# Kernel tuning notes

Measured on AMD Instinct MI355X. Metric: run time of the kernel, lower is better.

The kernel has to match this reference:

```python
import jax, jax.numpy as jnp
import numpy as np

N_PER_G = 100  # nodes per graph


def setup_inputs() -> dict:
    key = jax.random.key(0)
    ks = jax.random.split(key, 12)
    N, G, E = 100000, 1000, 1600000
    ninp, nout, K, H, H2 = 3, 10, 5, 64, 32
    x = jax.random.normal(ks[0], (N, ninp), jnp.float32)
    # within-graph random edges (contiguous node blocks per graph)
    epg = E // G
    gid = jnp.arange(E, dtype=jnp.int32) // epg
    src = jax.random.randint(ks[1], (E,), 0, N_PER_G, jnp.int32) + gid * N_PER_G
    dst = jax.random.randint(ks[2], (E,), 0, N_PER_G, jnp.int32) + gid * N_PER_G
    edge_index = jnp.stack([src, dst])
    batch = (jnp.arange(N, dtype=jnp.int32) // N_PER_G)
    lambda_max = 1.5 + 0.5 * jax.random.uniform(ks[3], (G,), jnp.float32)
    s = 0.05
    W1 = jax.random.normal(ks[4], (K, ninp, H), jnp.float32) * s
    b1 = jnp.zeros((H,), jnp.float32)
    W2 = jax.random.normal(ks[5], (K, H, H), jnp.float32) * s
    b2 = jnp.zeros((H,), jnp.float32)
    W3 = jax.random.normal(ks[6], (K, H, H), jnp.float32) * s
    b3 = jnp.zeros((H,), jnp.float32)
    bn_gamma = jnp.ones((H,), jnp.float32)
    bn_beta = jnp.zeros((H,), jnp.float32)
    bn_mean = jnp.zeros((H,), jnp.float32)
    bn_var = jnp.ones((H,), jnp.float32)
    fc1_w = jax.random.normal(ks[7], (H, H2), jnp.float32) * s
    fc1_b = jnp.zeros((H2,), jnp.float32)
    fc2_w = jax.random.normal(ks[8], (H2, nout), jnp.float32) * s
    fc2_b = jnp.zeros((nout,), jnp.float32)
    return dict(x=x, edge_index=edge_index, batch=batch, lambda_max=lambda_max,
                W1=W1, b1=b1, W2=W2, b2=b2, W3=W3, b3=b3,
                bn_gamma=bn_gamma, bn_beta=bn_beta, bn_mean=bn_mean, bn_var=bn_var,
                fc1_w=fc1_w, fc1_b=fc1_b, fc2_w=fc2_w, fc2_b=fc2_b)


def _cheb_conv(x, W, b, row, col, coef_edge, coef_loop):
    # PyG ChebConv with sym-normalized scaled Laplacian:
    # Lhat x = scatter_add(coef_edge * x[col] -> row) + coef_loop * x
    N = x.shape[0]
    def lhat(h):
        return jax.ops.segment_sum(coef_edge[:, None] * h[col], row,
                                   num_segments=N) + coef_loop[:, None] * h
    Tx0 = x
    out = Tx0 @ W[0]
    Tx1 = lhat(x)
    out = out + Tx1 @ W[1]
    for k in range(2, W.shape[0]):
        Tx2 = 2.0 * lhat(Tx1) - Tx0
        out = out + Tx2 @ W[k]
        Tx0, Tx1 = Tx1, Tx2
    return out + b


def reference(x, edge_index, batch, lambda_max,
              W1, b1, W2, b2, W3, b3,
              bn_gamma, bn_beta, bn_mean, bn_var,
              fc1_w, fc1_b, fc2_w, fc2_b):
    N = x.shape[0]
    G = lambda_max.shape[0]
    row, col = edge_index[0], edge_index[1]
    # sym Laplacian normalization, scaled by 2/lambda_max (per-graph)
    deg = jax.ops.segment_sum(jnp.ones_like(row, dtype=x.dtype), row, num_segments=N)
    dis = jnp.where(deg > 0, deg, 1.0) ** -0.5
    dis = jnp.where(deg > 0, dis, 0.0)
    lmax_e = lambda_max[batch[row]]
    coef_edge = -(2.0 / lmax_e) * dis[row] * dis[col]   # off-diagonal of Lhat
    coef_loop = 2.0 / lambda_max[batch] - 1.0           # diagonal of Lhat
    h = jax.nn.relu(_cheb_conv(x, W1, b1, row, col, coef_edge, coef_loop))
    h = jax.nn.relu(_cheb_conv(h, W2, b2, row, col, coef_edge, coef_loop))
    h = jax.nn.relu(_cheb_conv(h, W3, b3, row, col, coef_edge, coef_loop))
    # global mean pool over graphs
    sums = jax.ops.segment_sum(h, batch, num_segments=G)
    cnts = jax.ops.segment_sum(jnp.ones((N,), h.dtype), batch, num_segments=G)
    g = sums / jnp.maximum(cnts, 1.0)[:, None]
    # BatchNorm1d (eval mode, running stats), eps=1e-5
    g = (g - bn_mean) * jax.lax.rsqrt(bn_var + 1e-5) * bn_gamma + bn_beta
    g = jax.nn.relu(g @ fc1_w + fc1_b)
    return jax.nn.log_softmax(g @ fc2_w + fc2_b, axis=1)
```

## Files before the change

### kernel.cpp

```cpp
#include <hip/hip_runtime.h>

#define NPG 100
#define HF 64
#define SAT 136
#define CMW 29

typedef float  f4   __attribute__((ext_vector_type(4)));
typedef float  f16v __attribute__((ext_vector_type(16)));
typedef short  bf8  __attribute__((ext_vector_type(8)));

#define NB_T  (HF * SAT * 2)
#define OFF_MISC (2 * NB_T)
#define MISC_BYTES 2048
#define SMEM_BYTES (OFF_MISC + MISC_BYTES)

#define WT_TOTAL 46080

__device__ __forceinline__ unsigned short f2bf(float f) {
    unsigned u = __float_as_uint(f);
    u += 0x7fffu + ((u >> 16) & 1u);
    return (unsigned short)(u >> 16);
}
__device__ __forceinline__ unsigned cvt_pk_bf16(float lo, float hi) {
    unsigned r;
    asm("v_cvt_pk_bf16_f32 %0, %1, %2" : "=v"(r) : "v"(lo), "v"(hi));
    return r;
}
__device__ __forceinline__ f16v zerov16() {
    f16v z;
    #pragma unroll
    for (int i = 0; i < 16; i++) z[i] = 0.f;
    return z;
}

union BF8U { unsigned u[4]; bf8 b; };

__global__ void wconv(const float* __restrict__ W1, const float* __restrict__ W2,
                      const float* __restrict__ W3, unsigned short* __restrict__ ws)
{
    int idx = blockIdx.x * 256 + threadIdx.x;
    if (idx >= WT_TOTAL) return;
    float v;
    if (idx < 5120) {
        int k5 = idx >> 10, rem = idx & 1023, fo = rem >> 4, fi = rem & 15;
        v = (fi < 3) ? W1[(k5 * 3 + fi) * HF + fo] : 0.f;
    } else if (idx < 25600) {
        int j = idx - 5120;
        int k5 = j >> 12, rem = j & 4095, fo = rem >> 6, fi = rem & 63;
        v = W2[(k5 * HF + fi) * HF + fo];
    } else {
        int j = idx - 25600;
        int k5 = j >> 12, rem = j & 4095, fo = rem >> 6, fi = rem & 63;
        v = W3[(k5 * HF + fi) * HF + fo];
    }
    ws[idx] = f2bf(v);
}

__launch_bounds__(256, 2)
__global__ void chebreg(const float* __restrict__ x, const int* __restrict__ ei,
                        const float* __restrict__ lambda_max,
                        const unsigned short* __restrict__ Wt,
                        const float* __restrict__ b1, const float* __restrict__ b2,
                        const float* __restrict__ b3,
                        const float* __restrict__ bng, const float* __restrict__ bnb,
                        const float* __restrict__ bnm, const float* __restrict__ bnv,
                        const float* __restrict__ fc1w, const float* __restrict__ fc1b,
                        const float* __restrict__ fc2w, const float* __restrict__ fc2b,
                        float* __restrict__ out, int E_total, int epg)
{
    extern __shared__ char sm[];
    const int tid = threadIdx.x;
    const int g = blockIdx.x;
    const int ebase = g * epg, nbase = g * NPG;
    const int wg = tid >> 6, lane = tid & 63;
    const int l31 = lane & 31, hh = lane >> 5;
    const int nb = 32 * wg;
    const int np = nb + l31;
    const bool npv = (np < NPG);

    unsigned* Cm  = (unsigned*)sm;
    float* dis    = (float*)(sm + OFF_MISC);
    float* b_all  = (float*)(sm + OFF_MISC + 448);
    float* gvn    = (float*)(sm + OFF_MISC + 1216);
    float* zf     = (float*)(sm + OFF_MISC + 1472);
    float* logits = (float*)(sm + OFF_MISC + 1600);
    float* lsep   = (float*)(sm + OFF_MISC + 1664);

    const float lam = lambda_max[g];
    const float two_l = 2.0f / lam;
    const float cl = two_l - 1.0f;

    for (int i = tid; i < (128 * CMW) / 4; i += 256)
        ((f4*)Cm)[i] = (f4){0.f, 0.f, 0.f, 0.f};
    __syncthreads();
    for (int e = tid; e < epg; e += 256) {
        int r = ei[ebase + e] - nbase;
        int c = ei[E_total + ebase + e] - nbase;
        atomicAdd(&Cm[r * CMW + (c >> 2)], 1u << (8 * (c & 3)));
    }
    __syncthreads();
    if (tid < 112) {
        float dv = 0.f;
        if (tid < NPG) {
            unsigned s = 0;
            #pragma unroll
            for (int w = 0; w < 25; w++) {
                unsigned u = Cm[tid * CMW + w];
                s += (u & 255) + ((u >> 8) & 255) + ((u >> 16) & 255) + (u >> 24);
            }
            dv = s > 0 ? rsqrtf((float)s) : 0.f;
        }
        dis[tid] = dv;
    }
    if (tid < 192)
        b_all[tid] = (tid < 64) ? b1[tid] : (tid < 128) ? b2[tid - 64] : b3[tid - 128];
    __syncthreads();

    bf8 afT[7];
    {
        float base = npv ? (-two_l * dis[np]) : 0.f;
        #pragma unroll
        for (int Ks = 0; Ks < 7; Ks++) {
            int n0 = Ks * 16 + 8 * hh;
            unsigned w0 = npv ? Cm[np * CMW + (n0 >> 2)]     : 0u;
            unsigned w1 = npv ? Cm[np * CMW + (n0 >> 2) + 1] : 0u;
            float vv[8];
            #pragma unroll
            for (int j = 0; j < 8; j++) {
                int n = n0 + j;
                unsigned cnt = (((j < 4) ? w0 : w1) >> (8 * (n & 3))) & 255u;
                float v = base * (float)cnt * dis[n];
                if (npv && n == np) v += cl;
                vv[j] = v;
            }
            BF8U t;
            #pragma unroll
            for (int p = 0; p < 4; p++) t.u[p] = cvt_pk_bf16(vv[2 * p], vv[2 * p + 1]);
            afT[Ks] = t.b;
        }
    }
    __syncthreads();

    for (int i = tid; i < (2 * NB_T) / 16; i += 256)
        ((f4*)sm)[i] = (f4){0.f, 0.f, 0.f, 0.f};
    __syncthreads();

    unsigned prev[2][8], oldr[2][8];
    #pragma unroll
    for (int ct = 0; ct < 2; ct++)
        #pragma unroll
        for (int p = 0; p < 8; p++) prev[ct][p] = 0u;

    if (hh == 0 && npv) {
        float x0 = x[(nbase + np) * 3 + 0];
        float x1 = x[(nbase + np) * 3 + 1];
        float x2 = x[(nbase + np) * 3 + 2];
        prev[0][0] = cvt_pk_bf16(x0, x1);
        prev[0][1] = cvt_pk_bf16(x2, 0.f);
        *(unsigned short*)(sm + (0 * SAT + np) * 2) = (unsigned short)(prev[0][0] & 0xffff);
        *(unsigned short*)(sm + (1 * SAT + np) * 2) = (unsigned short)(prev[0][0] >> 16);
        *(unsigned short*)(sm + (2 * SAT + np) * 2) = (unsigned short)(prev[0][1] & 0xffff);
    }
    __syncthreads();

    f16v acc[2];
    int cur = 0;

    for (int L = 0; L < 3; L++) {
        const bool l0 = (L == 0);
        const unsigned short* Wl = l0 ? Wt : (Wt + (L == 1 ? 5120 : 25600));
        const int wstr = l0 ? 16 : 64;
        const int nKs  = l0 ? 1 : 4;
        acc[0] = zerov16();
        acc[1] = zerov16();

        auto TWreg = [&](int k5) {
            #pragma unroll
            for (int Ks = 0; Ks < 4; Ks++) {
                if (Ks < nKs) {
                    unsigned a0 = prev[Ks >> 1][4 * (Ks & 1) + 0];
                    unsigned b0 = prev[Ks >> 1][4 * (Ks & 1) + 2];
                    unsigned a1 = prev[Ks >> 1][4 * (Ks & 1) + 1];
                    unsigned b1v = prev[Ks >> 1][4 * (Ks & 1) + 3];
                    asm volatile("v_permlane32_swap_b32 %0, %1" : "+v"(a0), "+v"(b0));
                    asm volatile("v_permlane32_swap_b32 %0, %1" : "+v"(a1), "+v"(b1v));
                    BF8U bfr; bfr.u[0] = a0; bfr.u[1] = a1; bfr.u[2] = b0; bfr.u[3] = b1v;
                    #pragma unroll
                    for (int ct = 0; ct < 2; ct++) {
                        bf8 wf = *(const bf8*)(Wl + (k5 * 64 + 32 * ct + l31) * wstr
                                               + Ks * 16 + 8 * hh);
                        acc[ct] = __builtin_amdgcn_mfma_f32_32x32x16_bf16(wf, bfr.b, acc[ct], 0, 0, 0);
                    }
                }
            }
        };

        for (int s = 1; s <= 4; s++) {
            const char* bcur = sm + cur * NB_T;
            bf8 Af0[7], Af1[7];
            #pragma unroll
            for (int Ks = 0; Ks < 7; Ks++)
                Af0[Ks] = *(const bf8*)(bcur + ((0 + l31) * SAT + Ks * 16 + 8 * hh) * 2);
            if (!l0) {
                #pragma unroll
                for (int Ks = 0; Ks < 7; Ks++)
                    Af1[Ks] = *(const bf8*)(bcur + ((32 + l31) * SAT + Ks * 16 + 8 * hh) * 2);
            }
            f16v c0 = zerov16(), c1 = zerov16();
            #pragma unroll
            for (int Ks = 0; Ks < 7; Ks++)
                c0 = __builtin_amdgcn_mfma_f32_32x32x16_bf16(Af0[Ks], afT[Ks], c0, 0, 0, 0);
            if (!l0) {
                #pragma unroll
                for (int Ks = 0; Ks < 7; Ks++)
                    c1 = __builtin_amdgcn_mfma_f32_32x32x16_bf16(Af1[Ks], afT[Ks], c1, 0, 0, 0);
            }

            TWreg(s - 1);

            #pragma unroll
            for (int p = 0; p < 8; p++) {
                float ve = c0[2 * p], vo = c0[2 * p + 1];
                if (s >= 2) {
                    unsigned o = oldr[0][p];
                    ve = 2.f * ve - __uint_as_float(o << 16);
                    vo = 2.f * vo - __uint_as_float(o & 0xffff0000u);
                }
                oldr[0][p] = prev[0][p];
                prev[0][p] = cvt_pk_bf16(ve, vo);
            }
            if (!l0) {
                #pragma unroll
                for (int p = 0; p < 8; p++) {
                    float ve = c1[2 * p], vo = c1[2 * p + 1];
                    if (s >= 2) {
                        unsigned o = oldr[1][p];
                        ve = 2.f * ve - __uint_as_float(o << 16);
                        vo = 2.f * vo - __uint_as_float(o & 0xffff0000u);
                    }
                    oldr[1][p] = prev[1][p];
                    prev[1][p] = cvt_pk_bf16(ve, vo);
                }
            }

            if (s < 4) {
                char* bnx = sm + (cur ^ 1) * NB_T;
                if (l0) {
                    if (hh == 0) {
                        *(unsigned short*)(bnx + (0 * SAT + np) * 2) = (unsigned short)(prev[0][0] & 0xffff);
                        *(unsigned short*)(bnx + (1 * SAT + np) * 2) = (unsigned short)(prev[0][0] >> 16);
                        *(unsigned short*)(bnx + (2 * SAT + np) * 2) = (unsigned short)(prev[0][1] & 0xffff);
                    }
                } else {
                    #pragma unroll
                    for (int ct = 0; ct < 2; ct++) {
                        #pragma unroll
                        for (int p = 0; p < 8; p++) {
                            int fo = 32 * ct + ((2 * p) & 3) + 8 * (p >> 1) + 4 * hh;
                            *(unsigned short*)(bnx + (fo * SAT + np) * 2)       = (unsigned short)(prev[ct][p] & 0xffff);
                            *(unsigned short*)(bnx + ((fo + 1) * SAT + np) * 2) = (unsigned short)(prev[ct][p] >> 16);
                        }
                    }
                }
            }
            __syncthreads();
            cur ^= 1;
        }

        TWreg(4);

        if (L < 2) {
            const float* bl = b_all + L * 64;
            char* bt0 = sm + cur * NB_T;
            #pragma unroll
            for (int ct = 0; ct < 2; ct++) {
                #pragma unroll
                for (int p = 0; p < 8; p++) {
                    int fo = 32 * ct + ((2 * p) & 3) + 8 * (p >> 1) + 4 * hh;
                    float2 bb = *(const float2*)(bl + fo);
                    float ve = fmaxf(acc[ct][2 * p]     + bb.x, 0.f);
                    float vo = fmaxf(acc[ct][2 * p + 1] + bb.y, 0.f);
                    prev[ct][p] = cvt_pk_bf16(ve, vo);
                    *(unsigned short*)(bt0 + (fo * SAT + np) * 2)       = (unsigned short)(prev[ct][p] & 0xffff);
                    *(unsigned short*)(bt0 + ((fo + 1) * SAT + np) * 2) = (unsigned short)(prev[ct][p] >> 16);
                }
            }
            __syncthreads();
        } else {
            float* Sc = (float*)sm;
            const float* bl = b_all + 128;
            #pragma unroll
            for (int ct = 0; ct < 2; ct++) {
                #pragma unroll
                for (int p = 0; p < 8; p++) {
                    int fo = 32 * ct + ((2 * p) & 3) + 8 * (p >> 1) + 4 * hh;
                    float2 bb = *(const float2*)(bl + fo);
                    float ve = fmaxf(acc[ct][2 * p]     + bb.x, 0.f);
                    float vo = fmaxf(acc[ct][2 * p + 1] + bb.y, 0.f);
                    if (npv) {
                        Sc[fo * 132 + np]       = ve;
                        Sc[(fo + 1) * 132 + np] = vo;
                    }
                }
            }
            __syncthreads();
            if (tid < HF) {
                float ssum = 0.f;
                #pragma unroll
                for (int k = 0; k < 25; k++) {
                    f4 v = *(const f4*)(Sc + tid * 132 + 4 * k);
                    ssum += v[0] + v[1] + v[2] + v[3];
                }
                float gv = ssum * (1.0f / NPG);
                gv = (gv - bnm[tid]) * rsqrtf(bnv[tid] + 1e-5f) * bng[tid] + bnb[tid];
                gvn[tid] = gv;
            }
            __syncthreads();
        }
    }

    if (tid < 32) {
        float a = fc1b[tid];
        for (int f = 0; f < HF; f++) a += gvn[f] * fc1w[f * 32 + tid];
        zf[tid] = fmaxf(a, 0.f);
    }
    __syncthreads();
    if (tid < 10) {
        float a = fc2b[tid];
        for (int k = 0; k < 32; k++) a += zf[k] * fc2w[k * 10 + tid];
        logits[tid] = a;
    }
    __syncthreads();
    if (tid == 0) {
        float m = logits[0];
        for (int i = 1; i < 10; i++) m = fmaxf(m, logits[i]);
        float s = 0.f;
        for (int i = 0; i < 10; i++) s += expf(logits[i] - m);
        lsep[0] = m + logf(s);
    }
    __syncthreads();
    if (tid < 10) out[g * 10 + tid] = logits[tid] - lsep[0];
}

extern "C" void kernel_launch(void* const* d_in, const int* in_sizes, int n_in,
                              void* d_out, int out_size, void* d_ws, size_t ws_size,
                              hipStream_t stream) {
    const float* x    = (const float*)d_in[0];
    const int*   ei   = (const int*)d_in[1];
    const float* lmax = (const float*)d_in[3];
    const float* W1   = (const float*)d_in[4];
    const float* b1   = (const float*)d_in[5];
    const float* W2   = (const float*)d_in[6];
    const float* b2   = (const float*)d_in[7];
    const float* W3   = (const float*)d_in[8];
    const float* b3   = (const float*)d_in[9];
    const float* bng  = (const float*)d_in[10];
    const float* bnb  = (const float*)d_in[11];
    const float* bnm  = (const float*)d_in[12];
    const float* bnv  = (const float*)d_in[13];
    const float* fc1w = (const float*)d_in[14];
    const float* fc1b = (const float*)d_in[15];
    const float* fc2w = (const float*)d_in[16];
    const float* fc2b = (const float*)d_in[17];

    const int E = in_sizes[1] / 2;
    const int G = in_sizes[3];
    const int epg = E / G;

    unsigned short* Wt = (unsigned short*)d_ws;

    wconv<<<(WT_TOTAL + 255) / 256, 256, 0, stream>>>(W1, W2, W3, Wt);

    hipFuncSetAttribute((const void*)chebreg,
                        hipFuncAttributeMaxDynamicSharedMemorySize, SMEM_BYTES);

    chebreg<<<G, 256, SMEM_BYTES, stream>>>(x, ei, lmax, Wt, b1, b2, b3,
                                            bng, bnb, bnm, bnv, fc1w, fc1b, fc2w, fc2b,
                                            (float*)d_out, E, epg);
}
```

Before: 181.5 us.

## Split output feature halves across paired waves with 512-thread blocks

Doubles the block to 512 threads so each of the 8 waves owns one node tile and one 32-wide output-feature half, instead of 4 waves each computing both halves. Partner waves exchange their Chebyshev terms through a new shared-memory exchange buffer. The double-buffered T tile becomes a single buffer protected by an extra barrier per step. The aim is more wave parallelism per graph and lower per-wave register pressure, at the cost of more barriers, extra LDS traffic for the exchange, and a larger block that may cut blocks resident per CU.

```diff
diff --git a/kernel.cpp b/kernel.cpp
--- a/kernel.cpp
+++ b/kernel.cpp
@@ -4,15 +4,17 @@
 #define HF 64
 #define SAT 136
 #define CMW 29
+#define XBS 520
 
 typedef float  f4   __attribute__((ext_vector_type(4)));
 typedef float  f16v __attribute__((ext_vector_type(16)));
 typedef short  bf8  __attribute__((ext_vector_type(8)));
 
-#define NB_T  (HF * SAT * 2)
-#define OFF_MISC (2 * NB_T)
-#define MISC_BYTES 2048
-#define SMEM_BYTES (OFF_MISC + MISC_BYTES)
+#define SZ_TC   (HF * SAT * 2)
+#define OFF_XB  SZ_TC
+#define SZ_XB   (8 * XBS * 4)
+#define OFF_MISC (OFF_XB + SZ_XB)
+#define SMEM_BYTES (OFF_MISC + 2048)
 
 #define WT_TOTAL 46080
 
@@ -56,7 +58,7 @@
     ws[idx] = f2bf(v);
 }
 
-__launch_bounds__(256, 2)
+__launch_bounds__(512, 2)
 __global__ void chebreg(const float* __restrict__ x, const int* __restrict__ ei,
                         const float* __restrict__ lambda_max,
                         const unsigned short* __restrict__ Wt,
@@ -74,11 +76,14 @@
     const int ebase = g * epg, nbase = g * NPG;
     const int wg = tid >> 6, lane = tid & 63;
     const int l31 = lane & 31, hh = lane >> 5;
-    const int nb = 32 * wg;
+    const int tile = wg >> 1, ct = wg & 1;
+    const int nb = 32 * tile;
     const int np = nb + l31;
     const bool npv = (np < NPG);
+    const int foB = 32 * ct;
 
     unsigned* Cm  = (unsigned*)sm;
+    unsigned* xb  = (unsigned*)(sm + OFF_XB);
     float* dis    = (float*)(sm + OFF_MISC);
     float* b_all  = (float*)(sm + OFF_MISC + 448);
     float* gvn    = (float*)(sm + OFF_MISC + 1216);
@@ -86,14 +91,17 @@
     float* logits = (float*)(sm + OFF_MISC + 1600);
     float* lsep   = (float*)(sm + OFF_MISC + 1664);
 
+    const int xslot_me = wg * 64 + lane;
+    const int xslot_pa = (wg ^ 1) * 64 + lane;
+
     const float lam = lambda_max[g];
     const float two_l = 2.0f / lam;
     const float cl = two_l - 1.0f;
 
-    for (int i = tid; i < (128 * CMW) / 4; i += 256)
+    for (int i = tid; i < (128 * CMW) / 4; i += 512)
         ((f4*)Cm)[i] = (f4){0.f, 0.f, 0.f, 0.f};
     __syncthreads();
-    for (int e = tid; e < epg; e += 256) {
+    for (int e = tid; e < epg; e += 512) {
         int r = ei[ebase + e] - nbase;
         int c = ei[E_total + ebase + e] - nbase;
         atomicAdd(&Cm[r * CMW + (c >> 2)], 1u << (8 * (c & 3)));
@@ -141,166 +149,167 @@
     }
     __syncthreads();
 
-    for (int i = tid; i < (2 * NB_T) / 16; i += 256)
+    for (int i = tid; i < OFF_MISC / 16; i += 512)
         ((f4*)sm)[i] = (f4){0.f, 0.f, 0.f, 0.f};
     __syncthreads();
 
-    unsigned prev[2][8], oldr[2][8];
+    unsigned prev[8], oldr[8];
     #pragma unroll
-    for (int ct = 0; ct < 2; ct++)
-        #pragma unroll
-        for (int p = 0; p < 8; p++) prev[ct][p] = 0u;
-
-    if (hh == 0 && npv) {
+    for (int p = 0; p < 8; p++) prev[p] = 0u;
+
+    if (ct == 0 && hh == 0 && npv) {
         float x0 = x[(nbase + np) * 3 + 0];
         float x1 = x[(nbase + np) * 3 + 1];
         float x2 = x[(nbase + np) * 3 + 2];
-        prev[0][0] = cvt_pk_bf16(x0, x1);
-        prev[0][1] = cvt_pk_bf16(x2, 0.f);
-        *(unsigned short*)(sm + (0 * SAT + np) * 2) = (unsigned short)(prev[0][0] & 0xffff);
-        *(unsigned short*)(sm + (1 * SAT + np) * 2) = (unsigned short)(prev[0][0] >> 16);
-        *(unsigned short*)(sm + (2 * SAT + np) * 2) = (unsigned short)(prev[0][1] & 0xffff);
-    }
-    __syncthreads();
-
-    f16v acc[2];
-    int cur = 0;
+        prev[0] = cvt_pk_bf16(x0, x1);
+        prev[1] = cvt_pk_bf16(x2, 0.f);
+        *(unsigned short*)(sm + (0 * SAT + np) * 2) = (unsigned short)(prev[0] & 0xffff);
+        *(unsigned short*)(sm + (1 * SAT + np) * 2) = (unsigned short)(prev[0] >> 16);
+        *(unsigned short*)(sm + (2 * SAT + np) * 2) = (unsigned short)(prev[1] & 0xffff);
+    }
+    if (ct == 0) {
+        xb[0 * XBS + xslot_me] = prev[0];
+        xb[1 * XBS + xslot_me] = prev[1];
+    }
+    __syncthreads();
+
+    f16v acc;
 
     for (int L = 0; L < 3; L++) {
         const bool l0 = (L == 0);
         const unsigned short* Wl = l0 ? Wt : (Wt + (L == 1 ? 5120 : 25600));
         const int wstr = l0 ? 16 : 64;
         const int nKs  = l0 ? 1 : 4;
-        acc[0] = zerov16();
-        acc[1] = zerov16();
-
-        auto TWreg = [&](int k5) {
+        const bool doLH = !(l0 && ct == 1);
+        acc = zerov16();
+
+        auto TWK = [&](const unsigned (&fiLo)[8], const unsigned (&fiHi)[8], const int k5) {
             #pragma unroll
             for (int Ks = 0; Ks < 4; Ks++) {
                 if (Ks < nKs) {
-                    unsigned a0 = prev[Ks >> 1][4 * (Ks & 1) + 0];
-                    unsigned b0 = prev[Ks >> 1][4 * (Ks & 1) + 2];
-                    unsigned a1 = prev[Ks >> 1][4 * (Ks & 1) + 1];
-                    unsigned b1v = prev[Ks >> 1][4 * (Ks & 1) + 3];
+                    unsigned a0, b0, a1, b1v;
+                    if (Ks < 2) {
+                        a0 = fiLo[4 * (Ks & 1) + 0]; b0  = fiLo[4 * (Ks & 1) + 2];
+                        a1 = fiLo[4 * (Ks & 1) + 1]; b1v = fiLo[4 * (Ks & 1) + 3];
+                    } else {
+                        a0 = fiHi[4 * (Ks & 1) + 0]; b0  = fiHi[4 * (Ks & 1) + 2];
+                        a1 = fiHi[4 * (Ks & 1) + 1]; b1v = fiHi[4 * (Ks & 1) + 3];
+                    }
                     asm volatile("v_permlane32_swap_b32 %0, %1" : "+v"(a0), "+v"(b0));
                     asm volatile("v_permlane32_swap_b32 %0, %1" : "+v"(a1), "+v"(b1v));
                     BF8U bfr; bfr.u[0] = a0; bfr.u[1] = a1; bfr.u[2] = b0; bfr.u[3] = b1v;
-                    #pragma unroll
-                    for (int ct = 0; ct < 2; ct++) {
-                        bf8 wf = *(const bf8*)(Wl + (k5 * 64 + 32 * ct + l31) * wstr
-                                               + Ks * 16 + 8 * hh);
-                        acc[ct] = __builtin_amdgcn_mfma_f32_32x32x16_bf16(wf, bfr.b, acc[ct], 0, 0, 0);
-                    }
+                    bf8 wf = *(const bf8*)(Wl + (k5 * 64 + foB + l31) * wstr + Ks * 16 + 8 * hh);
+                    acc = __builtin_amdgcn_mfma_f32_32x32x16_bf16(wf, bfr.b, acc, 0, 0, 0);
                 }
             }
         };
 
         for (int s = 1; s <= 4; s++) {
-            const char* bcur = sm + cur * NB_T;
-            bf8 Af0[7], Af1[7];
-            #pragma unroll
-            for (int Ks = 0; Ks < 7; Ks++)
-                Af0[Ks] = *(const bf8*)(bcur + ((0 + l31) * SAT + Ks * 16 + 8 * hh) * 2);
-            if (!l0) {
+            unsigned prevP[8];
+            const int pl = l0 ? 4 : 8;
+            #pragma unroll
+            for (int p = 0; p < 8; p++)
+                if (p < pl) prevP[p] = xb[p * XBS + xslot_pa];
+
+            bf8 Af[7];
+            if (doLH) {
                 #pragma unroll
                 for (int Ks = 0; Ks < 7; Ks++)
-                    Af1[Ks] = *(const bf8*)(bcur + ((32 + l31) * SAT + Ks * 16 + 8 * hh) * 2);
-            }
-            f16v c0 = zerov16(), c1 = zerov16();
-            #pragma unroll
-            for (int Ks = 0; Ks < 7; Ks++)
-                c0 = __builtin_amdgcn_mfma_f32_32x32x16_bf16(Af0[Ks], afT[Ks], c0, 0, 0, 0);
-            if (!l0) {
+                    Af[Ks] = *(const bf8*)(sm + ((foB + l31) * SAT + Ks * 16 + 8 * hh) * 2);
+            }
+
+            if (ct == 0) TWK(prev, prevP, s - 1); else TWK(prevP, prev, s - 1);
+
+            if (doLH) {
+                f16v c = zerov16();
                 #pragma unroll
                 for (int Ks = 0; Ks < 7; Ks++)
-                    c1 = __builtin_amdgcn_mfma_f32_32x32x16_bf16(Af1[Ks], afT[Ks], c1, 0, 0, 0);
-            }
-
-            TWreg(s - 1);
-
-            #pragma unroll
-            for (int p = 0; p < 8; p++) {
-                float ve = c0[2 * p], vo = c0[2 * p + 1];
-                if (s >= 2) {
-                    unsigned o = oldr[0][p];
-                    ve = 2.f * ve - __uint_as_float(o << 16);
-                    vo = 2.f * vo - __uint_as_float(o & 0xffff0000u);
-                }
-                oldr[0][p] = prev[0][p];
-                prev[0][p] = cvt_pk_bf16(ve, vo);
-            }
-            if (!l0) {
+                    c = __builtin_amdgcn_mfma_f32_32x32x16_bf16(Af[Ks], afT[Ks], c, 0, 0, 0);
+                const int pmax = l0 ? 2 : 8;
                 #pragma unroll
                 for (int p = 0; p < 8; p++) {
-                    float ve = c1[2 * p], vo = c1[2 * p + 1];
-                    if (s >= 2) {
-                        unsigned o = oldr[1][p];
-                        ve = 2.f * ve - __uint_as_float(o << 16);
-                        vo = 2.f * vo - __uint_as_float(o & 0xffff0000u);
+                    if (p < pmax) {
+                        float ve = c[2 * p], vo = c[2 * p + 1];
+                        if (s >= 2) {
+                            unsigned o = oldr[p];
+                            ve = 2.f * ve - __uint_as_float(o << 16);
+                            vo = 2.f * vo - __uint_as_float(o & 0xffff0000u);
+                        }
+                        oldr[p] = prev[p];
+                        prev[p] = cvt_pk_bf16(ve, vo);
                     }
-                    oldr[1][p] = prev[1][p];
-                    prev[1][p] = cvt_pk_bf16(ve, vo);
-                }
-            }
-
-            if (s < 4) {
-                char* bnx = sm + (cur ^ 1) * NB_T;
+                }
+            }
+            __syncthreads();
+
+            if (doLH) {
+                if (s < 4) {
+                    if (l0) {
+                        if (hh == 0) {
+                            *(unsigned short*)(sm + (0 * SAT + np) * 2) = (unsigned short)(prev[0] & 0xffff);
+                            *(unsigned short*)(sm + (1 * SAT + np) * 2) = (unsigned short)(prev[0] >> 16);
+                            *(unsigned short*)(sm + (2 * SAT + np) * 2) = (unsigned short)(prev[1] & 0xffff);
+                        }
+                    } else {
+                        #pragma unroll
+                        for (int p = 0; p < 8; p++) {
+                            int fo = foB + ((2 * p) & 3) + 8 * (p >> 1) + 4 * hh;
+                            char* ad = sm + (fo * SAT + np) * 2;
+                            *(unsigned short*)ad = (unsigned short)(prev[p] & 0xffff);
+                            *(unsigned short*)(ad + SAT * 2) = (unsigned short)(prev[p] >> 16);
+                        }
+                    }
+                }
                 if (l0) {
-                    if (hh == 0) {
-                        *(unsigned short*)(bnx + (0 * SAT + np) * 2) = (unsigned short)(prev[0][0] & 0xffff);
-                        *(unsigned short*)(bnx + (1 * SAT + np) * 2) = (unsigned short)(prev[0][0] >> 16);
-                        *(unsigned short*)(bnx + (2 * SAT + np) * 2) = (unsigned short)(prev[0][1] & 0xffff);
-                    }
+                    xb[0 * XBS + xslot_me] = prev[0];
+                    xb[1 * XBS + xslot_me] = prev[1];
                 } else {
                     #pragma unroll
-                    for (int ct = 0; ct < 2; ct++) {
-                        #pragma unroll
-                        for (int p = 0; p < 8; p++) {
-                            int fo = 32 * ct + ((2 * p) & 3) + 8 * (p >> 1) + 4 * hh;
-                            *(unsigned short*)(bnx + (fo * SAT + np) * 2)       = (unsigned short)(prev[ct][p] & 0xffff);
-                            *(unsigned short*)(bnx + ((fo + 1) * SAT + np) * 2) = (unsigned short)(prev[ct][p] >> 16);
-                        }
-                    }
-                }
-            }
-            __syncthreads();
-            cur ^= 1;
-        }
-
-        TWreg(4);
+                    for (int p = 0; p < 8; p++)
+                        xb[p * XBS + xslot_me] = prev[p];
+                }
+            }
+            __syncthreads();
+        }
+
+        {
+            unsigned prevP[8];
+            const int pl = l0 ? 4 : 8;
+            #pragma unroll
+            for (int p = 0; p < 8; p++)
+                if (p < pl) prevP[p] = xb[p * XBS + xslot_pa];
+            if (ct == 0) TWK(prev, prevP, 4); else TWK(prevP, prev, 4);
+        }
 
         if (L < 2) {
+            __syncthreads();
             const float* bl = b_all + L * 64;
-            char* bt0 = sm + cur * NB_T;
-            #pragma unroll
-            for (int ct = 0; ct < 2; ct++) {
-                #pragma unroll
-                for (int p = 0; p < 8; p++) {
-                    int fo = 32 * ct + ((2 * p) & 3) + 8 * (p >> 1) + 4 * hh;
-                    float2 bb = *(const float2*)(bl + fo);
-                    float ve = fmaxf(acc[ct][2 * p]     + bb.x, 0.f);
-                    float vo = fmaxf(acc[ct][2 * p + 1] + bb.y, 0.f);
-                    prev[ct][p] = cvt_pk_bf16(ve, vo);
-                    *(unsigned short*)(bt0 + (fo * SAT + np) * 2)       = (unsigned short)(prev[ct][p] & 0xffff);
-                    *(unsigned short*)(bt0 + ((fo + 1) * SAT + np) * 2) = (unsigned short)(prev[ct][p] >> 16);
-                }
+            #pragma unroll
+            for (int p = 0; p < 8; p++) {
+                int fo = foB + ((2 * p) & 3) + 8 * (p >> 1) + 4 * hh;
+                float2 bb = *(const float2*)(bl + fo);
+                float ve = fmaxf(acc[2 * p]     + bb.x, 0.f);
+                float vo = fmaxf(acc[2 * p + 1] + bb.y, 0.f);
+                prev[p] = cvt_pk_bf16(ve, vo);
+                char* ad = sm + (fo * SAT + np) * 2;
+                *(unsigned short*)ad = (unsigned short)(prev[p] & 0xffff);
+                *(unsigned short*)(ad + SAT * 2) = (unsigned short)(prev[p] >> 16);
+                xb[p * XBS + xslot_me] = prev[p];
             }
             __syncthreads();
         } else {
+            __syncthreads();
             float* Sc = (float*)sm;
             const float* bl = b_all + 128;
             #pragma unroll
-            for (int ct = 0; ct < 2; ct++) {
-                #pragma unroll
-                for (int p = 0; p < 8; p++) {
-                    int fo = 32 * ct + ((2 * p) & 3) + 8 * (p >> 1) + 4 * hh;
-                    float2 bb = *(const float2*)(bl + fo);
-                    float ve = fmaxf(acc[ct][2 * p]     + bb.x, 0.f);
-                    float vo = fmaxf(acc[ct][2 * p + 1] + bb.y, 0.f);
-                    if (npv) {
-                        Sc[fo * 132 + np]       = ve;
-                        Sc[(fo + 1) * 132 + np] = vo;
-                    }
+            for (int p = 0; p < 8; p++) {
+                int fo = foB + ((2 * p) & 3) + 8 * (p >> 1) + 4 * hh;
+                float2 bb = *(const float2*)(bl + fo);
+                float ve = fmaxf(acc[2 * p]     + bb.x, 0.f);
+                float vo = fmaxf(acc[2 * p + 1] + bb.y, 0.f);
+                if (npv) {
+                    Sc[fo * 132 + np]       = ve;
+                    Sc[(fo + 1) * 132 + np] = vo;
                 }
             }
             __syncthreads();
@@ -374,7 +383,7 @@
     hipFuncSetAttribute((const void*)chebreg,
                         hipFuncAttributeMaxDynamicSharedMemorySize, SMEM_BYTES);
 
-    chebreg<<<G, 256, SMEM_BYTES, stream>>>(x, ei, lmax, Wt, b1, b2, b3,
+    chebreg<<<G, 512, SMEM_BYTES, stream>>>(x, ei, lmax, Wt, b1, b2, b3,
                                             bng, bnb, bnm, bnv, fc1w, fc1b, fc2w, fc2b,
                                             (float*)d_out, E, epg);
 }
```

Result: slower. 226.2 us (+24.6%).

## Cut block barriers by merging setup phases and finishing the head in one wavefront

Applied to the files above, without the earlier changes.

Gives the count matrix its own LDS region so it and the ping-pong T buffers can be zeroed in a single pass. Degree is now counted with atomics in the edge loop, so the separate degree-reduction phase and bias staging go away, and x is loaded before zeroing. The Chebyshev step now issues the weight MFMAs before the Laplacian MFMAs and handles the two column tiles in a loop. The pooling and MLP head run inside one wavefront with lgkmcnt waits instead of block-wide barriers. This trades a larger LDS footprint, which may lower occupancy, and extra atomic traffic for fewer __syncthreads.

```diff
diff --git a/kernel.cpp b/kernel.cpp
--- a/kernel.cpp
+++ b/kernel.cpp
@@ -9,10 +9,11 @@
 typedef float  f16v __attribute__((ext_vector_type(16)));
 typedef short  bf8  __attribute__((ext_vector_type(8)));
 
-#define NB_T  (HF * SAT * 2)
-#define OFF_MISC (2 * NB_T)
-#define MISC_BYTES 2048
-#define SMEM_BYTES (OFF_MISC + MISC_BYTES)
+#define SZ_TC   (HF * SAT * 2)
+#define OFF_CM  (2 * SZ_TC)
+#define CMBYTES (128 * CMW * 4)
+#define OFF_MISC (OFF_CM + CMBYTES)
+#define SMEM_BYTES (OFF_MISC + 1280)
 
 #define WT_TOTAL 46080
 
@@ -31,6 +32,14 @@
     #pragma unroll
     for (int i = 0; i < 16; i++) z[i] = 0.f;
     return z;
+}
+__device__ __forceinline__ void bar_lgkm() {
+    asm volatile("s_waitcnt lgkmcnt(0)" ::: "memory");
+    __builtin_amdgcn_s_barrier();
+    __builtin_amdgcn_sched_barrier(0);
+}
+__device__ __forceinline__ void wait_lgkm() {
+    asm volatile("s_waitcnt lgkmcnt(0)" ::: "memory");
 }
 
 union BF8U { unsigned u[4]; bf8 b; };
@@ -74,51 +83,57 @@
     const int ebase = g * epg, nbase = g * NPG;
     const int wg = tid >> 6, lane = tid & 63;
     const int l31 = lane & 31, hh = lane >> 5;
-    const int nb = 32 * wg;
-    const int np = nb + l31;
+    const int np = 32 * wg + l31;
     const bool npv = (np < NPG);
 
-    unsigned* Cm  = (unsigned*)sm;
-    float* dis    = (float*)(sm + OFF_MISC);
-    float* b_all  = (float*)(sm + OFF_MISC + 448);
-    float* gvn    = (float*)(sm + OFF_MISC + 1216);
-    float* zf     = (float*)(sm + OFF_MISC + 1472);
-    float* logits = (float*)(sm + OFF_MISC + 1600);
-    float* lsep   = (float*)(sm + OFF_MISC + 1664);
+    unsigned* Cm   = (unsigned*)(sm + OFF_CM);
+    unsigned* deg  = (unsigned*)(sm + OFF_MISC);
+    float* gvn     = (float*)(sm + OFF_MISC + 448);
+    float* zf      = (float*)(sm + OFF_MISC + 704);
+    float* logits  = (float*)(sm + OFF_MISC + 832);
+    float* lsep    = (float*)(sm + OFF_MISC + 896);
 
     const float lam = lambda_max[g];
     const float two_l = 2.0f / lam;
     const float cl = two_l - 1.0f;
 
-    for (int i = tid; i < (128 * CMW) / 4; i += 256)
-        ((f4*)Cm)[i] = (f4){0.f, 0.f, 0.f, 0.f};
-    __syncthreads();
+    float xr0 = 0.f, xr1 = 0.f, xr2 = 0.f;
+    if (hh == 0 && npv) {
+        xr0 = x[(nbase + np) * 3 + 0];
+        xr1 = x[(nbase + np) * 3 + 1];
+        xr2 = x[(nbase + np) * 3 + 2];
+    }
+
+    for (int i = tid; i < (2 * SZ_TC + CMBYTES) / 16; i += 256)
+        ((f4*)sm)[i] = (f4){0.f, 0.f, 0.f, 0.f};
+    if (tid < 112) deg[tid] = 0u;
+    bar_lgkm();
+
     for (int e = tid; e < epg; e += 256) {
         int r = ei[ebase + e] - nbase;
         int c = ei[E_total + ebase + e] - nbase;
         atomicAdd(&Cm[r * CMW + (c >> 2)], 1u << (8 * (c & 3)));
-    }
-    __syncthreads();
-    if (tid < 112) {
-        float dv = 0.f;
-        if (tid < NPG) {
-            unsigned s = 0;
-            #pragma unroll
-            for (int w = 0; w < 25; w++) {
-                unsigned u = Cm[tid * CMW + w];
-                s += (u & 255) + ((u >> 8) & 255) + ((u >> 16) & 255) + (u >> 24);
-            }
-            dv = s > 0 ? rsqrtf((float)s) : 0.f;
-        }
-        dis[tid] = dv;
-    }
-    if (tid < 192)
-        b_all[tid] = (tid < 64) ? b1[tid] : (tid < 128) ? b2[tid - 64] : b3[tid - 128];
-    __syncthreads();
+        atomicAdd(&deg[r], 1u);
+    }
+    unsigned prev[2][8], oldr[2][8];
+    #pragma unroll
+    for (int ct = 0; ct < 2; ct++)
+        #pragma unroll
+        for (int p = 0; p < 8; p++) { prev[ct][p] = 0u; oldr[ct][p] = 0u; }
+    if (hh == 0 && npv) {
+        prev[0][0] = cvt_pk_bf16(xr0, xr1);
+        prev[0][1] = cvt_pk_bf16(xr2, 0.f);
+        *(unsigned short*)(sm + (0 * SAT + np) * 2) = (unsigned short)(prev[0][0] & 0xffff);
+        *(unsigned short*)(sm + (1 * SAT + np) * 2) = (unsigned short)(prev[0][0] >> 16);
+        *(unsigned short*)(sm + (2 * SAT + np) * 2) = (unsigned short)(prev[0][1] & 0xffff);
+    }
+    bar_lgkm();
 
     bf8 afT[7];
     {
-        float base = npv ? (-two_l * dis[np]) : 0.f;
+        unsigned dgr = npv ? deg[np] : 0u;
+        float disr = dgr ? rsqrtf((float)dgr) : 0.f;
+        const float base = npv ? (-two_l * disr) : 0.f;
         #pragma unroll
         for (int Ks = 0; Ks < 7; Ks++) {
             int n0 = Ks * 16 + 8 * hh;
@@ -128,8 +143,10 @@
             #pragma unroll
             for (int j = 0; j < 8; j++) {
                 int n = n0 + j;
+                unsigned dg = deg[n];
+                float dv = dg ? rsqrtf((float)dg) : 0.f;
                 unsigned cnt = (((j < 4) ? w0 : w1) >> (8 * (n & 3))) & 255u;
-                float v = base * (float)cnt * dis[n];
+                float v = base * (float)cnt * dv;
                 if (npv && n == np) v += cl;
                 vv[j] = v;
             }
@@ -139,48 +156,26 @@
             afT[Ks] = t.b;
         }
     }
-    __syncthreads();
-
-    for (int i = tid; i < (2 * NB_T) / 16; i += 256)
-        ((f4*)sm)[i] = (f4){0.f, 0.f, 0.f, 0.f};
-    __syncthreads();
-
-    unsigned prev[2][8], oldr[2][8];
-    #pragma unroll
-    for (int ct = 0; ct < 2; ct++)
-        #pragma unroll
-        for (int p = 0; p < 8; p++) prev[ct][p] = 0u;
-
-    if (hh == 0 && npv) {
-        float x0 = x[(nbase + np) * 3 + 0];
-        float x1 = x[(nbase + np) * 3 + 1];
-        float x2 = x[(nbase + np) * 3 + 2];
-        prev[0][0] = cvt_pk_bf16(x0, x1);
-        prev[0][1] = cvt_pk_bf16(x2, 0.f);
-        *(unsigned short*)(sm + (0 * SAT + np) * 2) = (unsigned short)(prev[0][0] & 0xffff);
-        *(unsigned short*)(sm + (1 * SAT + np) * 2) = (unsigned short)(prev[0][0] >> 16);
-        *(unsigned short*)(sm + (2 * SAT + np) * 2) = (unsigned short)(prev[0][1] & 0xffff);
-    }
-    __syncthreads();
 
     f16v acc[2];
-    int cur = 0;
+    const float* bsv[3] = {b1, b2, b3};
 
     for (int L = 0; L < 3; L++) {
         const bool l0 = (L == 0);
         const unsigned short* Wl = l0 ? Wt : (Wt + (L == 1 ? 5120 : 25600));
         const int wstr = l0 ? 16 : 64;
         const int nKs  = l0 ? 1 : 4;
+        const int pb = L & 1;
         acc[0] = zerov16();
         acc[1] = zerov16();
 
-        auto TWreg = [&](int k5) {
+        auto TWK = [&](int k5) {
             #pragma unroll
             for (int Ks = 0; Ks < 4; Ks++) {
                 if (Ks < nKs) {
-                    unsigned a0 = prev[Ks >> 1][4 * (Ks & 1) + 0];
-                    unsigned b0 = prev[Ks >> 1][4 * (Ks & 1) + 2];
-                    unsigned a1 = prev[Ks >> 1][4 * (Ks & 1) + 1];
+                    unsigned a0  = prev[Ks >> 1][4 * (Ks & 1) + 0];
+                    unsigned b0  = prev[Ks >> 1][4 * (Ks & 1) + 2];
+                    unsigned a1  = prev[Ks >> 1][4 * (Ks & 1) + 1];
                     unsigned b1v = prev[Ks >> 1][4 * (Ks & 1) + 3];
                     asm volatile("v_permlane32_swap_b32 %0, %1" : "+v"(a0), "+v"(b0));
                     asm volatile("v_permlane32_swap_b32 %0, %1" : "+v"(a1), "+v"(b1v));
@@ -196,82 +191,62 @@
         };
 
         for (int s = 1; s <= 4; s++) {
-            const char* bcur = sm + cur * NB_T;
-            bf8 Af0[7], Af1[7];
-            #pragma unroll
-            for (int Ks = 0; Ks < 7; Ks++)
-                Af0[Ks] = *(const bf8*)(bcur + ((0 + l31) * SAT + Ks * 16 + 8 * hh) * 2);
-            if (!l0) {
+            const int rp = (pb + s - 1) & 1, wp = rp ^ 1;
+            const char* tcR = sm + rp * SZ_TC;
+            char* tcW = sm + wp * SZ_TC;
+
+            TWK(s - 1);
+
+            #pragma unroll
+            for (int ct = 0; ct < 2; ct++) {
+                if (l0 && ct == 1) continue;
+                f16v c = zerov16();
                 #pragma unroll
-                for (int Ks = 0; Ks < 7; Ks++)
-                    Af1[Ks] = *(const bf8*)(bcur + ((32 + l31) * SAT + Ks * 16 + 8 * hh) * 2);
-            }
-            f16v c0 = zerov16(), c1 = zerov16();
-            #pragma unroll
-            for (int Ks = 0; Ks < 7; Ks++)
-                c0 = __builtin_amdgcn_mfma_f32_32x32x16_bf16(Af0[Ks], afT[Ks], c0, 0, 0, 0);
-            if (!l0) {
-                #pragma unroll
-                for (int Ks = 0; Ks < 7; Ks++)
-                    c1 = __builtin_amdgcn_mfma_f32_32x32x16_bf16(Af1[Ks], afT[Ks], c1, 0, 0, 0);
-            }
-
-            TWreg(s - 1);
-
-            #pragma unroll
-            for (int p = 0; p < 8; p++) {
-                float ve = c0[2 * p], vo = c0[2 * p + 1];
-                if (s >= 2) {
-                    unsigned o = oldr[0][p];
-                    ve = 2.f * ve - __uint_as_float(o << 16);
-                    vo = 2.f * vo - __uint_as_float(o & 0xffff0000u);
-                }
-                oldr[0][p] = prev[0][p];
-                prev[0][p] = cvt_pk_bf16(ve, vo);
-            }
-            if (!l0) {
+                for (int Ks = 0; Ks < 7; Ks++) {
+                    bf8 A = *(const bf8*)(tcR + ((32 * ct + l31) * SAT + Ks * 16 + 8 * hh) * 2);
+                    c = __builtin_amdgcn_mfma_f32_32x32x16_bf16(A, afT[Ks], c, 0, 0, 0);
+                }
+                const int pmax = l0 ? 2 : 8;
                 #pragma unroll
                 for (int p = 0; p < 8; p++) {
-                    float ve = c1[2 * p], vo = c1[2 * p + 1];
-                    if (s >= 2) {
-                        unsigned o = oldr[1][p];
-                        ve = 2.f * ve - __uint_as_float(o << 16);
-                        vo = 2.f * vo - __uint_as_float(o & 0xffff0000u);
+                    if (p < pmax) {
+                        float ve = c[2 * p], vo = c[2 * p + 1];
+                        if (s >= 2) {
+                            unsigned o = oldr[ct][p];
+                            ve = 2.f * ve - __uint_as_float(o << 16);
+                            vo = 2.f * vo - __uint_as_float(o & 0xffff0000u);
+                        }
+                        oldr[ct][p] = prev[ct][p];
+                        prev[ct][p] = cvt_pk_bf16(ve, vo);
                     }
-                    oldr[1][p] = prev[1][p];
-                    prev[1][p] = cvt_pk_bf16(ve, vo);
-                }
-            }
-
-            if (s < 4) {
-                char* bnx = sm + (cur ^ 1) * NB_T;
-                if (l0) {
-                    if (hh == 0) {
-                        *(unsigned short*)(bnx + (0 * SAT + np) * 2) = (unsigned short)(prev[0][0] & 0xffff);
-                        *(unsigned short*)(bnx + (1 * SAT + np) * 2) = (unsigned short)(prev[0][0] >> 16);
-                        *(unsigned short*)(bnx + (2 * SAT + np) * 2) = (unsigned short)(prev[0][1] & 0xffff);
-                    }
-                } else {
-                    #pragma unroll
-                    for (int ct = 0; ct < 2; ct++) {
+                }
+                if (s < 4) {
+                    if (l0) {
+                        if (hh == 0) {
+                            *(unsigned short*)(tcW + (0 * SAT + np) * 2) = (unsigned short)(prev[0][0] & 0xffff);
+                            *(unsigned short*)(tcW + (1 * SAT + np) * 2) = (unsigned short)(prev[0][0] >> 16);
+                            *(unsigned short*)(tcW + (2 * SAT + np) * 2) = (unsigned short)(prev[0][1] & 0xffff);
+                        }
+                    } else {
                         #pragma unroll
                         for (int p = 0; p < 8; p++) {
                             int fo = 32 * ct + ((2 * p) & 3) + 8 * (p >> 1) + 4 * hh;
-                            *(unsigned short*)(bnx + (fo * SAT + np) * 2)       = (unsigned short)(prev[ct][p] & 0xffff);
-                            *(unsigned short*)(bnx + ((fo + 1) * SAT + np) * 2) = (unsigned short)(prev[ct][p] >> 16);
+                            char* ad = tcW + (fo * SAT + np) * 2;
+                            *(unsigned short*)ad = (unsigned short)(prev[ct][p] & 0xffff);
+                            *(unsigned short*)(ad + SAT * 2) = (unsigned short)(prev[ct][p] >> 16);
                         }
                     }
                 }
             }
-            __syncthreads();
-            cur ^= 1;
-        }
-
-        TWreg(4);
+            bar_lgkm();
+        }
+
+        TWK(4);
 
         if (L < 2) {
-            const float* bl = b_all + L * 64;
-            char* bt0 = sm + cur * NB_T;
+            const int op = pb ^ 1;
+            char* tcW = sm + op * SZ_TC;
+            const float* bl = bsv[L];
             #pragma unroll
             for (int ct = 0; ct < 2; ct++) {
                 #pragma unroll
@@ -281,14 +256,15 @@
                     float ve = fmaxf(acc[ct][2 * p]     + bb.x, 0.f);
                     float vo = fmaxf(acc[ct][2 * p + 1] + bb.y, 0.f);
                     prev[ct][p] = cvt_pk_bf16(ve, vo);
-                    *(unsigned short*)(bt0 + (fo * SAT + np) * 2)       = (unsigned short)(prev[ct][p] & 0xffff);
-                    *(unsigned short*)(bt0 + ((fo + 1) * SAT + np) * 2) = (unsigned short)(prev[ct][p] >> 16);
-                }
-            }
-            __syncthreads();
+                    char* ad = tcW + (fo * SAT + np) * 2;
+                    *(unsigned short*)ad = (unsigned short)(prev[ct][p] & 0xffff);
+                    *(unsigned short*)(ad + SAT * 2) = (unsigned short)(prev[ct][p] >> 16);
+                }
+            }
+            bar_lgkm();
         } else {
             float* Sc = (float*)sm;
-            const float* bl = b_all + 128;
+            const float* bl = bsv[2];
             #pragma unroll
             for (int ct = 0; ct < 2; ct++) {
                 #pragma unroll
@@ -303,43 +279,44 @@
                     }
                 }
             }
-            __syncthreads();
-            if (tid < HF) {
-                float ssum = 0.f;
-                #pragma unroll
-                for (int k = 0; k < 25; k++) {
-                    f4 v = *(const f4*)(Sc + tid * 132 + 4 * k);
-                    ssum += v[0] + v[1] + v[2] + v[3];
-                }
-                float gv = ssum * (1.0f / NPG);
-                gv = (gv - bnm[tid]) * rsqrtf(bnv[tid] + 1e-5f) * bng[tid] + bnb[tid];
-                gvn[tid] = gv;
-            }
-            __syncthreads();
-        }
-    }
-
-    if (tid < 32) {
-        float a = fc1b[tid];
-        for (int f = 0; f < HF; f++) a += gvn[f] * fc1w[f * 32 + tid];
-        zf[tid] = fmaxf(a, 0.f);
-    }
-    __syncthreads();
-    if (tid < 10) {
-        float a = fc2b[tid];
-        for (int k = 0; k < 32; k++) a += zf[k] * fc2w[k * 10 + tid];
-        logits[tid] = a;
-    }
-    __syncthreads();
-    if (tid == 0) {
-        float m = logits[0];
-        for (int i = 1; i < 10; i++) m = fmaxf(m, logits[i]);
-        float s = 0.f;
-        for (int i = 0; i < 10; i++) s += expf(logits[i] - m);
-        lsep[0] = m + logf(s);
-    }
-    __syncthreads();
-    if (tid < 10) out[g * 10 + tid] = logits[tid] - lsep[0];
+            bar_lgkm();
+        }
+    }
+
+    if (wg == 0) {
+        const float* Sc = (const float*)sm;
+        float ssum = 0.f;
+        #pragma unroll
+        for (int k = 0; k < 25; k++) {
+            f4 v = *(const f4*)(Sc + lane * 132 + 4 * k);
+            ssum += v[0] + v[1] + v[2] + v[3];
+        }
+        float gv = ssum * (1.0f / NPG);
+        gv = (gv - bnm[lane]) * rsqrtf(bnv[lane] + 1e-5f) * bng[lane] + bnb[lane];
+        gvn[lane] = gv;
+        wait_lgkm();
+        if (lane < 32) {
+            float a = fc1b[lane];
+            for (int f = 0; f < HF; f++) a += gvn[f] * fc1w[f * 32 + lane];
+            zf[lane] = fmaxf(a, 0.f);
+        }
+        wait_lgkm();
+        if (lane < 10) {
+            float a = fc2b[lane];
+            for (int k = 0; k < 32; k++) a += zf[k] * fc2w[k * 10 + lane];
+            logits[lane] = a;
+        }
+        wait_lgkm();
+        if (lane == 0) {
+            float m = logits[0];
+            for (int i = 1; i < 10; i++) m = fmaxf(m, logits[i]);
+            float s = 0.f;
+            for (int i = 0; i < 10; i++) s += expf(logits[i] - m);
+            lsep[0] = m + logf(s);
+        }
+        wait_lgkm();
+        if (lane < 10) out[g * 10 + lane] = logits[lane] - lsep[0];
+    }
 }
 
 extern "C" void kernel_launch(void* const* d_in, const int* in_sizes, int n_in,
```

Result: faster. 172.0 us (-5.2%).
